# Optimization experiments

Hardware: AMD Instinct MI355X
Metric: run time of the kernel (lower is better)

Reference implementation:

```python
import jax, jax.numpy as jnp
import numpy as np

NUM_HEADS = 8
KEY_DIM = 32   # head_dim * attn_ratio(=1.0); head_dim = 256 // 8
SCALE = KEY_DIM ** -0.5


def qconv(x, w, groups, pad):
    """Quaternion (Hamilton product) conv. x: [B,C,4,H,W], w: [4,O,C//groups,kh,kw]."""
    B, C, Q, H, W = x.shape
    # fold the 4 quaternion components into the batch dim -> one conv per weight component
    xs = jnp.transpose(x, (0, 2, 1, 3, 4)).reshape(B * 4, C, H, W)
    ys = []
    for i in range(4):
        y = jax.lax.conv_general_dilated(
            xs, w[i], (1, 1), [(pad, pad), (pad, pad)],
            dimension_numbers=('NCHW', 'OIHW', 'NCHW'), feature_group_count=groups)
        ys.append(y.reshape(B, 4, y.shape[1], y.shape[2], y.shape[3]))
    yr, yi, yj, yk = ys  # y{w}[:, a] = conv(x_component_a, w_component_w)
    out_r = yr[:, 0] - yi[:, 1] - yj[:, 2] - yk[:, 3]
    out_i = yi[:, 0] + yr[:, 1] + yk[:, 2] - yj[:, 3]
    out_j = yj[:, 0] - yk[:, 1] + yr[:, 2] + yi[:, 3]
    out_k = yk[:, 0] + yj[:, 1] - yi[:, 2] + yr[:, 3]
    return jnp.stack([out_r, out_i, out_j, out_k], axis=2)  # [B,O,4,H,W]


def iqbn(x, gamma, beta, eps=1e-5):
    """Independent quaternion BN: per (channel, component) stats over (B,H,W)."""
    mean = x.mean(axis=(0, 3, 4), keepdims=True)
    var = x.var(axis=(0, 3, 4), keepdims=True)
    g = gamma[None, :, :, None, None]
    b = beta[None, :, :, None, None]
    return g * (x - mean) * jax.lax.rsqrt(var + eps) + b


def psablock(x, w_qkv, w_proj, w_pe, g_n, b_n, w_f1, g_f1, b_f1, w_f2, g_f2, b_f2):
    B, C, Q, H, W = x.shape
    N = H * W
    # --- QAttention ---
    qkv = qconv(x, w_qkv, 1, 0).reshape(B, NUM_HEADS, -1, 4, N)  # [B,nh,2kd+hd,4,N]
    q = qkv[:, :, :KEY_DIM]
    k = qkv[:, :, KEY_DIM:2 * KEY_DIM]
    v = qkv[:, :, 2 * KEY_DIM:]
    # channel attention: gram over spatial tokens N, softmax over channel dim d
    attn = jnp.einsum('bhcqn,bhdqn->bhqcd', q, k) * SCALE
    attn = jax.nn.softmax(attn, axis=-1)
    o = jnp.einsum('bhqcd,bhdqn->bhcqn', attn, v).reshape(B, C, 4, H, W)
    o = o + qconv(o, w_pe, C // 4, 1)   # depthwise-style 3x3 positional conv
    o = qconv(o, w_proj, 1, 0)
    o = iqbn(o, g_n, b_n)
    x = x + o  # shortcut
    # --- conv FFN ---
    f = qconv(x, w_f1, 1, 0)
    f = jax.nn.relu(iqbn(f, g_f1, b_f1))
    f = qconv(f, w_f2, 1, 0)
    f = iqbn(f, g_f2, b_f2)
    return x + f  # shortcut


def setup_inputs() -> dict:
    key = jax.random.key(0)
    ks = jax.random.split(key, 6)
    C, S = 256, 64
    return {
        'x': jax.random.normal(ks[0], (4, C, 4, S, S), jnp.float32),
        'w_qkv': jax.random.normal(ks[1], (4, 3 * C, C, 1, 1), jnp.float32) * 0.05,
        'w_proj': jax.random.normal(ks[2], (4, C, C, 1, 1), jnp.float32) * 0.05,
        'w_pe': jax.random.normal(ks[3], (4, C, 4, 3, 3), jnp.float32) * 0.05,
        'g_n': jnp.ones((C, 4), jnp.float32),
        'b_n': jnp.zeros((C, 4), jnp.float32),
        'w_f1': jax.random.normal(ks[4], (4, 2 * C, C, 1, 1), jnp.float32) * 0.05,
        'g_f1': jnp.ones((2 * C, 4), jnp.float32),
        'b_f1': jnp.zeros((2 * C, 4), jnp.float32),
        'w_f2': jax.random.normal(ks[5], (4, C, 2 * C, 1, 1), jnp.float32) * 0.05,
        'g_f2': jnp.ones((C, 4), jnp.float32),
        'b_f2': jnp.zeros((C, 4), jnp.float32),
    }


def reference(x, w_qkv, w_proj, w_pe, g_n, b_n, w_f1, g_f1, b_f1, w_f2, g_f2, b_f2):
    return psablock(x, w_qkv, w_proj, w_pe, g_n, b_n, w_f1, g_f1, b_f1, w_f2, g_f2, b_f2)
```

## Files before the change

### kernel.cpp

```cpp
#include <hip/hip_runtime.h>

typedef unsigned short u16;
typedef __bf16 bf16x8 __attribute__((ext_vector_type(8)));
typedef float f32x4 __attribute__((ext_vector_type(4)));

typedef const __attribute__((address_space(1))) void gv_t;
typedef __attribute__((address_space(3))) void lv_t;

__device__ __forceinline__ float b2f(u16 u) {
    union { unsigned int i; float f; } v; v.i = ((unsigned int)u) << 16; return v.f;
}
__device__ __forceinline__ u16 f2b(float f) {
    union { unsigned int i; float f; } v; v.f = f;
    unsigned int b = v.i;
    return (u16)((b + 0x7FFFu + ((b >> 16) & 1u)) >> 16);
}

__constant__ int   c_qidx[16] = {0,1,2,3, 1,0,3,2, 2,3,0,1, 3,2,1,0};
__constant__ float c_qsgn[16] = {1,-1,-1,-1, 1,1,1,-1, 1,-1,1,1, 1,1,-1,1};

__device__ __forceinline__ void frag_decode(long i, int KT, int& m, int& k) {
    int j = (int)(i & 7), r16 = (int)((i >> 3) & 15);
    int quad = (int)((i >> 7) & 3), frag = (int)((i >> 9) & 7);
    long t2 = i >> 12;
    int ktile = (int)(t2 % KT), mtile = (int)(t2 / KT);
    m = mtile * 128 + frag * 16 + r16;
    k = ktile * 32 + quad * 8 + j;
}
__device__ __forceinline__ u16 weff(const float* __restrict__ w, int OC, int Cin, int m, int k) {
    int o = m >> 2, p = m & 3, c = k >> 2, q = k & 3, pq = (p << 2) | q;
    return f2b(c_qsgn[pq] * w[c_qidx[pq] * OC + o * Cin + c]);
}

__global__ void build_weights(const float* __restrict__ wqkv, const float* __restrict__ wproj,
                              const float* __restrict__ wf1, const float* __restrict__ wf2,
                              const float* __restrict__ wpe,
                              u16* __restrict__ Wq, u16* __restrict__ Wp, u16* __restrict__ W1,
                              u16* __restrict__ W2, float* __restrict__ Wpe_eff)
{
    long i = (long)blockIdx.x * 256 + threadIdx.x;
    int m, k;
    if (i < 3145728L) {
        frag_decode(i, 32, m, k);
        Wq[i] = weff(wqkv, 196608, 256, m, k);
        return;
    }
    i -= 3145728L;
    if (i < 1048576L) {
        frag_decode(i, 32, m, k);
        Wp[i] = weff(wproj, 65536, 256, m, k);
        return;
    }
    i -= 1048576L;
    if (i < 2097152L) {
        frag_decode(i, 32, m, k);
        W1[i] = weff(wf1, 131072, 256, m, k);
        return;
    }
    i -= 2097152L;
    if (i < 2097152L) {
        frag_decode(i, 64, m, k);
        W2[i] = weff(wf2, 131072, 512, m, k);
        return;
    }
    i -= 2097152L;
    if (i < 147456L) {
        int g = (int)(i / 2304), r = (int)(i % 2304);
        int tap = r >> 8, r2 = r & 255;
        int fi = r2 >> 4, of = r2 & 15;
        int ol = of >> 2, p = of & 3, ci = fi >> 2, q = fi & 3, pq = (p << 2) | q;
        Wpe_eff[i] = c_qsgn[pq] * wpe[c_qidx[pq] * 9216 + (g * 4 + ol) * 36 + ci * 9 + tap];
    }
}

__global__ void zero_f(float* __restrict__ a)
{
    a[blockIdx.x * 256 + threadIdx.x] = 0.f;
}

__global__ __launch_bounds__(256) void cast_tr(const float* __restrict__ x, u16* __restrict__ Xt)
{
    int b = blockIdx.z, mt = blockIdx.y * 64, nt = blockIdx.x * 64;
    __shared__ u16 tl[64][66];
    int t = threadIdx.x, sub = t >> 4, c4 = (t & 15) * 4;
#pragma unroll
    for (int rr = 0; rr < 4; rr++) {
        int row = rr * 16 + sub;
        float4 v = *(const float4*)(x + ((long)b * 1024 + mt + row) * 4096 + nt + c4);
        uint2 pk;
        pk.x = (unsigned int)f2b(v.x) | ((unsigned int)f2b(v.y) << 16);
        pk.y = (unsigned int)f2b(v.z) | ((unsigned int)f2b(v.w) << 16);
        *(uint2*)(&tl[row][c4]) = pk;
    }
    __syncthreads();
#pragma unroll
    for (int rr = 0; rr < 4; rr++) {
        int row = rr * 16 + sub;
        uint2 o;
        o.x = (unsigned int)tl[c4][row] | ((unsigned int)tl[c4 + 1][row] << 16);
        o.y = (unsigned int)tl[c4 + 2][row] | ((unsigned int)tl[c4 + 3][row] << 16);
        *(uint2*)(Xt + ((long)b * 4096 + nt + row) * 1024 + mt + c4) = o;
    }
}

__device__ __forceinline__ void gl16(const u16* g, u16* l) {
    __builtin_amdgcn_global_load_lds((gv_t*)g, (lv_t*)l, 16, 0, 0);
}

template<int QM>
__device__ __forceinline__ void load_a(const u16* aS, bf16x8 (&afr)[4][2]) {
#pragma unroll
    for (int f = 0; f < 4; f++)
#pragma unroll
        for (int kk = 0; kk < 2; kk++)
            afr[f][kk] = *(const bf16x8*)(aS + (kk * 8 + QM * 4 + f) * 512);
}
template<int QN>
__device__ __forceinline__ void load_b(const u16* bS, bf16x8 (&bfr)[2][2]) {
#pragma unroll
    for (int g = 0; g < 2; g++)
#pragma unroll
        for (int kk = 0; kk < 2; kk++)
            bfr[g][kk] = *(const bf16x8*)(bS + (QN * 2 + g) * 1024 + kk * 512);
}
template<int QM, int QN>
__device__ __forceinline__ void mf16(const bf16x8 (&afr)[4][2], const bf16x8 (&bfr)[2][2],
                                     f32x4 (&acc)[8][4]) {
    __builtin_amdgcn_s_setprio(1);
#pragma unroll
    for (int f = 0; f < 4; f++)
#pragma unroll
        for (int g = 0; g < 2; g++)
#pragma unroll
            for (int kk = 0; kk < 2; kk++)
                acc[QM * 4 + f][QN * 2 + g] = __builtin_amdgcn_mfma_f32_16x16x32_bf16(
                    afr[f][kk], bfr[g][kk], acc[QM * 4 + f][QN * 2 + g], 0, 0, 0);
    __builtin_amdgcn_s_setprio(0);
}

template<bool TROUT>
__global__ __launch_bounds__(512, 2) void gemm256(
    const u16* __restrict__ A, const u16* __restrict__ Bt, u16* __restrict__ C,
    int M, int N, int K, long strideB, long strideC)
{
    __shared__ __align__(16) u16 smem[65536];
    const int t = threadIdx.x;
    const int b = blockIdx.z;
    const int m0 = blockIdx.y * 256, n0 = blockIdx.x * 256;
    const int l = t & 63, w = t >> 6;
    const int wr = w >> 2, wc = w & 3;
    const int quad = l >> 4, r16 = l & 15;
    const int KT32 = K >> 5, NT = K >> 6;
    const u16* Bb = Bt + (long)b * strideB;

    const u16* aB0 = A + (long)(2 * blockIdx.y) * KT32 * 4096 + t * 8;
    const u16* aB1 = aB0 + (long)KT32 * 4096;
    const int rowS = (w >> 1) * 16 + r16;
    const int colS = (w & 1) * 32 + quad * 8;
    const u16* bB0 = Bb + (long)(n0 + rowS) * K + colS;
    const u16* bB1 = bB0 + (long)128 * K;
    const long bStep = (long)64 * K;

#define STAGE_A(ktv, h) { \
    const u16* s_ = ((h) ? aB1 : aB0) + (long)(ktv) * 8192; \
    u16* d_ = smem + (((ktv) & 1) * 32768) + (h) * 8192 + t * 8; \
    gl16(s_, d_); gl16(s_ + 4096, d_ + 4096); }
#define STAGE_B(ktv, h) { \
    const u16* s_ = ((h) ? bB1 : bB0) + (ktv) * 64; \
    u16* d_ = smem + (((ktv) & 1) * 32768) + 16384 + (h) * 8192 + t * 8; \
    gl16(s_, d_); gl16(s_ + bStep, d_ + 4096); }
#define STAGE_TILE(ktv) { STAGE_A(ktv, 0); STAGE_A(ktv, 1); STAGE_B(ktv, 0); STAGE_B(ktv, 1); }

    STAGE_TILE(0);

    f32x4 acc[8][4];
#pragma unroll
    for (int i = 0; i < 8; i++)
#pragma unroll
        for (int j = 0; j < 4; j++) acc[i][j] = (f32x4){0.f, 0.f, 0.f, 0.f};

    for (int kt = 0; kt < NT; ++kt) {
        const int so = (kt & 1) * 32768;
        const u16* aS = smem + so + wr * 8192 + l * 8;
        const u16* bS = smem + so + 16384 + wc * 4096 + l * 8;
        bf16x8 afr[4][2], bfr[2][2];

        if (kt + 1 < NT) {
            STAGE_TILE(kt + 1);
            asm volatile("s_waitcnt vmcnt(8)" ::: "memory");
        } else {
            asm volatile("s_waitcnt vmcnt(0)" ::: "memory");
        }
        __builtin_amdgcn_s_barrier();

        load_a<0>(aS, afr);
        load_b<0>(bS, bfr);
        mf16<0, 0>(afr, bfr, acc);
        load_b<1>(bS, bfr);
        mf16<0, 1>(afr, bfr, acc);
        load_a<1>(aS, afr);
        mf16<1, 1>(afr, bfr, acc);
        load_b<0>(bS, bfr);
        mf16<1, 0>(afr, bfr, acc);

        __builtin_amdgcn_s_barrier();
    }
#undef STAGE_A
#undef STAGE_B
#undef STAGE_TILE

    if (!TROUT) {
        u16* Cb = C + (long)b * strideC;
#pragma unroll
        for (int i = 0; i < 8; i++)
#pragma unroll
            for (int j = 0; j < 4; j++) {
                int mm = m0 + wr * 128 + i * 16 + quad * 4;
                int nn = n0 + wc * 64 + j * 16 + r16;
#pragma unroll
                for (int r = 0; r < 4; r++)
                    Cb[(long)(mm + r) * N + nn] = f2b(acc[i][j][r]);
            }
    } else {
        u16* Ct = smem;
        u16* Cb = C + (long)b * strideC;
#pragma unroll
        for (int h = 0; h < 2; h++) {
            __syncthreads();
            if ((wc >> 1) == h) {
#pragma unroll
                for (int i = 0; i < 8; i++)
#pragma unroll
                    for (int j = 0; j < 4; j++) {
                        int nn = (wc & 1) * 64 + j * 16 + r16;
                        int mm = wr * 128 + i * 16 + quad * 4;
                        ushort4 pk;
                        pk.x = f2b(acc[i][j][0]); pk.y = f2b(acc[i][j][1]);
                        pk.z = f2b(acc[i][j][2]); pk.w = f2b(acc[i][j][3]);
                        *(ushort4*)(Ct + nn * 264 + mm) = pk;
                    }
            }
            __syncthreads();
#pragma unroll
            for (int e = 0; e < 8; e++) {
                int idx = e * 512 + t;
                int n = idx >> 5, m8 = (idx & 31) * 8;
                uint4 v = *(const uint4*)(Ct + n * 264 + m8);
                *(uint4*)(Cb + (long)(n0 + h * 128 + n) * M + m0 + m8) = v;
            }
        }
    }
}

__global__ __launch_bounds__(256) void attn_s(const u16* __restrict__ QKV, float* __restrict__ S)
{
    const int chunk = blockIdx.x, bhp = blockIdx.y;
    const int bi = bhp >> 5, h = (bhp >> 2) & 7, p = bhp & 3;
    const long rs = 16384;
    const u16* base = QKV + (long)bi * (3072L * 4096) + (long)(h * 384 + p) * 4096;
    const int t = threadIdx.x, l = t & 63, w = t >> 6;
    const int quad = l >> 4, r16 = l & 15;
    __shared__ float Sred[4][32][32];

    f32x4 acc[2][2];
#pragma unroll
    for (int i = 0; i < 2; i++)
#pragma unroll
        for (int j = 0; j < 2; j++) acc[i][j] = (f32x4){0.f, 0.f, 0.f, 0.f};

    const int nb = chunk * 1024 + w * 256 + quad * 8;
    for (int kk = 0; kk < 256; kk += 32) {
        long off = nb + kk;
        bf16x8 q0 = *(const bf16x8*)(base + (long)r16 * rs + off);
        bf16x8 q1 = *(const bf16x8*)(base + (long)(16 + r16) * rs + off);
        bf16x8 k0 = *(const bf16x8*)(base + (long)(32 + r16) * rs + off);
        bf16x8 k1 = *(const bf16x8*)(base + (long)(48 + r16) * rs + off);
        acc[0][0] = __builtin_amdgcn_mfma_f32_16x16x32_bf16(q0, k0, acc[0][0], 0, 0, 0);
        acc[0][1] = __builtin_amdgcn_mfma_f32_16x16x32_bf16(q0, k1, acc[0][1], 0, 0, 0);
        acc[1][0] = __builtin_amdgcn_mfma_f32_16x16x32_bf16(q1, k0, acc[1][0], 0, 0, 0);
        acc[1][1] = __builtin_amdgcn_mfma_f32_16x16x32_bf16(q1, k1, acc[1][1], 0, 0, 0);
    }
#pragma unroll
    for (int i = 0; i < 2; i++)
#pragma unroll
        for (int j = 0; j < 2; j++)
#pragma unroll
            for (int r = 0; r < 4; r++)
                Sred[w][i * 16 + quad * 4 + r][j * 16 + r16] = acc[i][j][r];
    __syncthreads();
    for (int e = t; e < 1024; e += 256) {
        int c = e >> 5, d = e & 31;
        float v = Sred[0][c][d] + Sred[1][c][d] + Sred[2][c][d] + Sred[3][c][d];
        atomicAdd(&S[(long)bhp * 1024 + e], v);
    }
}

__global__ __launch_bounds__(64) void attn_soft(float* __restrict__ S)
{
    const int bhp = blockIdx.x, t = threadIdx.x;
    if (t >= 32) return;
    float* row = S + (long)bhp * 1024 + t * 32;
    float r[32];
    float mx = -1e30f;
#pragma unroll
    for (int d = 0; d < 32; d++) { r[d] = row[d] * 0.17677669529663687f; mx = fmaxf(mx, r[d]); }
    float sum = 0.f;
#pragma unroll
    for (int d = 0; d < 32; d++) { r[d] = __expf(r[d] - mx); sum += r[d]; }
    float inv = 1.f / sum;
#pragma unroll
    for (int d = 0; d < 32; d++) row[d] = r[d] * inv;
}

__global__ __launch_bounds__(256) void attn_pv(const u16* __restrict__ QKV, const float* __restrict__ S,
                                               u16* __restrict__ O)
{
    const int ns = blockIdx.x * 512, bhp = blockIdx.y;
    const int bi = bhp >> 5, h = (bhp >> 2) & 7, p = bhp & 3;
    const long rs = 16384;
    const u16* base = QKV + (long)bi * (3072L * 4096) + (long)(h * 384 + p) * 4096;
    const int t = threadIdx.x;
    __shared__ float Pl[1024];
    for (int e = t; e < 1024; e += 256) Pl[e] = S[(long)bhp * 1024 + e];
    __syncthreads();

    float v[32][2];
#pragma unroll
    for (int d = 0; d < 32; d++) {
        unsigned int u = *(const unsigned int*)(base + (long)(64 + d) * rs + ns + 2 * t);
        v[d][0] = b2f((u16)u); v[d][1] = b2f((u16)(u >> 16));
    }
    u16* Ob = O + (long)bi * (1024L * 4096) + (long)(h * 128 + p) * 4096;
    for (int c = 0; c < 32; c++) {
        float s0 = 0.f, s1 = 0.f;
        const float4* prow = (const float4*)(&Pl[c * 32]);
#pragma unroll
        for (int dq = 0; dq < 8; dq++) {
            float4 pv = prow[dq];
            s0 = fmaf(pv.x, v[4*dq+0][0], s0); s1 = fmaf(pv.x, v[4*dq+0][1], s1);
            s0 = fmaf(pv.y, v[4*dq+1][0], s0); s1 = fmaf(pv.y, v[4*dq+1][1], s1);
            s0 = fmaf(pv.z, v[4*dq+2][0], s0); s1 = fmaf(pv.z, v[4*dq+2][1], s1);
            s0 = fmaf(pv.w, v[4*dq+3][0], s0); s1 = fmaf(pv.w, v[4*dq+3][1], s1);
        }
        *(unsigned int*)(Ob + (long)c * 16384 + ns + 2 * t) =
            (unsigned int)f2b(s0) | ((unsigned int)f2b(s1) << 16);
    }
}

__global__ __launch_bounds__(256) void pe_kernel(const u16* __restrict__ Oin,
                                                 const float* __restrict__ Wpe,
                                                 u16* __restrict__ O2t)
{
    const int tile = blockIdx.x, g = blockIdx.y, bi = blockIdx.z;
    const int y0 = (tile >> 2) * 16, x0 = (tile & 3) * 16;
    __shared__ float tin[16][324];
    const int t = threadIdx.x;
    const u16* Ob = Oin + (long)bi * (1024L * 4096) + (long)(g * 16) * 4096;
    for (int e = t; e < 16 * 324; e += 256) {
        int f = e / 324, rem = e % 324;
        int yy = rem / 18 - 1 + y0, xx = rem % 18 - 1 + x0;
        float v = 0.f;
        if (yy >= 0 && yy < 64 && xx >= 0 && xx < 64)
            v = b2f(Ob[(long)f * 4096 + yy * 64 + xx]);
        tin[f][rem] = v;
    }
    __syncthreads();
    const int y = t >> 4, x = t & 15;
    float acc[16];
#pragma unroll
    for (int of = 0; of < 16; of++) acc[of] = tin[of][(y + 1) * 18 + (x + 1)];
    const float* Wg = Wpe + g * 2304;
    for (int dy = 0; dy < 3; dy++)
        for (int dx = 0; dx < 3; dx++) {
            int off = (y + dy) * 18 + (x + dx);
            int tap = dy * 3 + dx;
            for (int fi = 0; fi < 16; fi++) {
                float v = tin[fi][off];
                const float* wp = Wg + (tap * 16 + fi) * 16;
#pragma unroll
                for (int of = 0; of < 16; of++) acc[of] = fmaf(wp[of], v, acc[of]);
            }
        }
    long n = (long)(y0 + y) * 64 + (x0 + x);
    unsigned int* op = (unsigned int*)(O2t + ((long)bi * 4096 + n) * 1024 + g * 16);
#pragma unroll
    for (int u = 0; u < 8; u++)
        op[u] = (unsigned int)f2b(acc[2 * u]) | ((unsigned int)f2b(acc[2 * u + 1]) << 16);
}

__global__ __launch_bounds__(256) void bn_stats(const u16* __restrict__ X, float* __restrict__ stats, int M)
{
    const int m = blockIdx.x, t = threadIdx.x;
    float s = 0.f, ss = 0.f;
    for (int b = 0; b < 4; b++) {
        const u16* rowp = X + ((long)b * M + m) * 4096;
        for (int pass = 0; pass < 2; pass++) {
            uint4 uv = *(const uint4*)(rowp + pass * 2048 + t * 8);
            unsigned int wsa[4] = {uv.x, uv.y, uv.z, uv.w};
#pragma unroll
            for (int u = 0; u < 4; u++) {
                float v0 = b2f((u16)wsa[u]), v1 = b2f((u16)(wsa[u] >> 16));
                s += v0 + v1; ss += v0 * v0 + v1 * v1;
            }
        }
    }
    __shared__ float rs[4], rss[4];
    for (int o = 32; o > 0; o >>= 1) { s += __shfl_down(s, o); ss += __shfl_down(ss, o); }
    if ((t & 63) == 0) { rs[t >> 6] = s; rss[t >> 6] = ss; }
    __syncthreads();
    if (t == 0) {
        float S = rs[0] + rs[1] + rs[2] + rs[3];
        float SS = rss[0] + rss[1] + rss[2] + rss[3];
        float mean = S * (1.f / 16384.f);
        float var = SS * (1.f / 16384.f) - mean * mean;
        stats[2 * m] = mean;
        stats[2 * m + 1] = rsqrtf(var + 1e-5f);
    }
}

__global__ __launch_bounds__(256) void bn_add_tr(const float* __restrict__ x, const u16* __restrict__ P,
    const float* __restrict__ stats, const float* __restrict__ gamma, const float* __restrict__ beta,
    u16* __restrict__ X1t)
{
    int b = blockIdx.z, mt = blockIdx.y * 64, nt = blockIdx.x * 64;
    __shared__ u16 tl[64][66];
    int t = threadIdx.x, sub = t >> 4, c4 = (t & 15) * 4;
#pragma unroll
    for (int rr = 0; rr < 4; rr++) {
        int row = rr * 16 + sub, m = mt + row;
        float gm = gamma[m] * stats[2 * m + 1];
        float bs = beta[m] - gm * stats[2 * m];
        long gi = ((long)b * 1024 + m) * 4096 + nt + c4;
        float4 xv = *(const float4*)(x + gi);
        uint2 pv = *(const uint2*)(P + gi);
        uint2 pk;
        pk.x = (unsigned int)f2b(xv.x + fmaf(gm, b2f((u16)pv.x), bs)) |
               ((unsigned int)f2b(xv.y + fmaf(gm, b2f((u16)(pv.x >> 16)), bs)) << 16);
        pk.y = (unsigned int)f2b(xv.z + fmaf(gm, b2f((u16)pv.y), bs)) |
               ((unsigned int)f2b(xv.w + fmaf(gm, b2f((u16)(pv.y >> 16)), bs)) << 16);
        *(uint2*)(&tl[row][c4]) = pk;
    }
    __syncthreads();
#pragma unroll
    for (int rr = 0; rr < 4; rr++) {
        int row = rr * 16 + sub;
        uint2 o;
        o.x = (unsigned int)tl[c4][row] | ((unsigned int)tl[c4 + 1][row] << 16);
        o.y = (unsigned int)tl[c4 + 2][row] | ((unsigned int)tl[c4 + 3][row] << 16);
        *(uint2*)(X1t + ((long)b * 4096 + nt + row) * 1024 + mt + c4) = o;
    }
}

__global__ __launch_bounds__(256) void bn_stats_col(const u16* __restrict__ Xp, float* __restrict__ accum)
{
    const int t = threadIdx.x;
    const int f0 = t * 8;
    float s[8], ss[8];
#pragma unroll
    for (int u = 0; u < 8; u++) { s[u] = 0.f; ss[u] = 0.f; }
    const u16* base = Xp + (long)blockIdx.x * 128 * 2048;
    for (int r = 0; r < 128; r++) {
        uint4 uv = *(const uint4*)(base + (long)r * 2048 + f0);
        unsigned int wsa[4] = {uv.x, uv.y, uv.z, uv.w};
#pragma unroll
        for (int u = 0; u < 4; u++) {
            float v0 = b2f((u16)wsa[u]), v1 = b2f((u16)(wsa[u] >> 16));
            s[2*u] += v0;   ss[2*u]   += v0 * v0;
            s[2*u+1] += v1; ss[2*u+1] += v1 * v1;
        }
    }
#pragma unroll
    for (int u = 0; u < 8; u++) {
        atomicAdd(&accum[f0 + u], s[u]);
        atomicAdd(&accum[2048 + f0 + u], ss[u]);
    }
}

__global__ __launch_bounds__(256) void bn_relu_ip(u16* __restrict__ Xp, const float* __restrict__ accum,
    const float* __restrict__ gamma, const float* __restrict__ beta)
{
    long i = ((long)blockIdx.x * 256 + threadIdx.x) * 8;
    int f = (int)(i & 2047);
    uint4 uv = *(const uint4*)(Xp + i);
    unsigned int wsa[4] = {uv.x, uv.y, uv.z, uv.w};
    unsigned int ov[4];
#pragma unroll
    for (int u = 0; u < 4; u++) {
        unsigned int o = 0;
#pragma unroll
        for (int h = 0; h < 2; h++) {
            int ff = f + 2 * u + h;
            float S = accum[ff], SS = accum[2048 + ff];
            float mean = S * (1.f / 16384.f);
            float var = SS * (1.f / 16384.f) - mean * mean;
            float g = gamma[ff] * rsqrtf(var + 1e-5f);
            float bb = beta[ff] - g * mean;
            float xv = b2f((u16)(wsa[u] >> (16 * h)));
            float v = fmaxf(fmaf(g, xv, bb), 0.f);
            o |= ((unsigned int)f2b(v)) << (16 * h);
        }
        ov[u] = o;
    }
    *(uint4*)(Xp + i) = *(uint4*)ov;
}

__global__ __launch_bounds__(256) void final_tr(const u16* __restrict__ X1t, const u16* __restrict__ F2,
    const float* __restrict__ stats, const float* __restrict__ gamma, const float* __restrict__ beta,
    float* __restrict__ out)
{
    int b = blockIdx.z, mt = blockIdx.y * 64, nt = blockIdx.x * 64;
    __shared__ u16 tl[64][66];
    int t = threadIdx.x, sub = t >> 4, c4 = (t & 15) * 4;
#pragma unroll
    for (int rr = 0; rr < 4; rr++) {
        int row = rr * 16 + sub;
        uint2 v = *(const uint2*)(X1t + ((long)b * 4096 + nt + row) * 1024 + mt + c4);
        *(uint2*)(&tl[row][c4]) = v;
    }
    __syncthreads();
#pragma unroll
    for (int rr = 0; rr < 4; rr++) {
        int row = rr * 16 + sub, m = mt + row;
        float gm = gamma[m] * stats[2 * m + 1];
        float bs = beta[m] - gm * stats[2 * m];
        long gi = ((long)b * 1024 + m) * 4096 + nt + c4;
        uint2 f = *(const uint2*)(F2 + gi);
        float4 o;
        o.x = b2f(tl[c4][row])     + fmaf(gm, b2f((u16)f.x), bs);
        o.y = b2f(tl[c4 + 1][row]) + fmaf(gm, b2f((u16)(f.x >> 16)), bs);
        o.z = b2f(tl[c4 + 2][row]) + fmaf(gm, b2f((u16)f.y), bs);
        o.w = b2f(tl[c4 + 3][row]) + fmaf(gm, b2f((u16)(f.y >> 16)), bs);
        *(float4*)(out + gi) = o;
    }
}

extern "C" void kernel_launch(void* const* d_in, const int* in_sizes, int n_in,
                              void* d_out, int out_size, void* d_ws, size_t ws_size,
                              hipStream_t stream)
{
    const float* x     = (const float*)d_in[0];
    const float* wqkv  = (const float*)d_in[1];
    const float* wproj = (const float*)d_in[2];
    const float* wpe   = (const float*)d_in[3];
    const float* g_n   = (const float*)d_in[4];
    const float* b_n   = (const float*)d_in[5];
    const float* wf1   = (const float*)d_in[6];
    const float* g_f1  = (const float*)d_in[7];
    const float* b_f1  = (const float*)d_in[8];
    const float* wf2   = (const float*)d_in[9];
    const float* g_f2  = (const float*)d_in[10];
    const float* b_f2  = (const float*)d_in[11];
    float* out = (float*)d_out;
    char* ws = (char*)d_ws;

    u16*   Wq      = (u16*)(ws + 0);
    u16*   Wp      = (u16*)(ws + 6291456);
    u16*   W1      = (u16*)(ws + 8388608);
    u16*   W2      = (u16*)(ws + 12582912);
    float* Wpe_eff = (float*)(ws + 16777216);
    float* st1     = (float*)(ws + 17367040);
    float* accum2  = (float*)(ws + 17375232);
    float* Sbuf    = (float*)(ws + 17391616);
    float* st3     = (float*)(ws + 17915904);
    u16*   QKV = (u16*)(ws + 17924096);
    u16*   O2t = (u16*)(ws + 17924096);
    u16*   X1t = (u16*)(ws + 17924096);
    u16*   P   = (u16*)(ws + 51478528);
    u16*   F1p = (u16*)(ws + 51478528);
    u16*   Xt  = (u16*)(ws + 118587392);
    u16*   Oat = (u16*)(ws + 118587392);
    u16*   F2  = (u16*)(ws + 118587392);

    zero_f<<<528, 256, 0, stream>>>(accum2);
    build_weights<<<33344, 256, 0, stream>>>(wqkv, wproj, wf1, wf2, wpe, Wq, Wp, W1, W2, Wpe_eff);
    cast_tr<<<dim3(64, 16, 4), 256, 0, stream>>>(x, Xt);
    gemm256<false><<<dim3(16, 12, 4), 512, 0, stream>>>(Wq, Xt, QKV, 3072, 4096, 1024, 4096L * 1024, 3072L * 4096);
    attn_s<<<dim3(4, 128), 256, 0, stream>>>(QKV, Sbuf);
    attn_soft<<<128, 64, 0, stream>>>(Sbuf);
    attn_pv<<<dim3(8, 128), 256, 0, stream>>>(QKV, Sbuf, Oat);
    pe_kernel<<<dim3(16, 64, 4), 256, 0, stream>>>(Oat, Wpe_eff, O2t);
    gemm256<false><<<dim3(16, 4, 4), 512, 0, stream>>>(Wp, O2t, P, 1024, 4096, 1024, 4096L * 1024, 1024L * 4096);
    bn_stats<<<1024, 256, 0, stream>>>(P, st1, 1024);
    bn_add_tr<<<dim3(64, 16, 4), 256, 0, stream>>>(x, P, st1, g_n, b_n, X1t);
    gemm256<true><<<dim3(16, 8, 4), 512, 0, stream>>>(W1, X1t, F1p, 2048, 4096, 1024, 4096L * 1024, 4096L * 2048);
    bn_stats_col<<<128, 256, 0, stream>>>(F1p, accum2);
    bn_relu_ip<<<16384, 256, 0, stream>>>(F1p, accum2, g_f1, b_f1);
    gemm256<false><<<dim3(16, 4, 4), 512, 0, stream>>>(W2, F1p, F2, 1024, 4096, 2048, 4096L * 2048, 1024L * 4096);
    bn_stats<<<1024, 256, 0, stream>>>(F2, st3, 1024);
    final_tr<<<dim3(64, 16, 4), 256, 0, stream>>>(X1t, F2, st3, g_f2, b_f2, out);
}
```

Measured before the change: 698.0 us.

## Software-pipeline LDS fragment reads across k-tiles in 256x256 GEMM

```diff
diff --git a/kernel.cpp b/kernel.cpp
--- a/kernel.cpp
+++ b/kernel.cpp
@@ -105,37 +105,6 @@
 
 __device__ __forceinline__ void gl16(const u16* g, u16* l) {
     __builtin_amdgcn_global_load_lds((gv_t*)g, (lv_t*)l, 16, 0, 0);
-}
-
-template<int QM>
-__device__ __forceinline__ void load_a(const u16* aS, bf16x8 (&afr)[4][2]) {
-#pragma unroll
-    for (int f = 0; f < 4; f++)
-#pragma unroll
-        for (int kk = 0; kk < 2; kk++)
-            afr[f][kk] = *(const bf16x8*)(aS + (kk * 8 + QM * 4 + f) * 512);
-}
-template<int QN>
-__device__ __forceinline__ void load_b(const u16* bS, bf16x8 (&bfr)[2][2]) {
-#pragma unroll
-    for (int g = 0; g < 2; g++)
-#pragma unroll
-        for (int kk = 0; kk < 2; kk++)
-            bfr[g][kk] = *(const bf16x8*)(bS + (QN * 2 + g) * 1024 + kk * 512);
-}
-template<int QM, int QN>
-__device__ __forceinline__ void mf16(const bf16x8 (&afr)[4][2], const bf16x8 (&bfr)[2][2],
-                                     f32x4 (&acc)[8][4]) {
-    __builtin_amdgcn_s_setprio(1);
-#pragma unroll
-    for (int f = 0; f < 4; f++)
-#pragma unroll
-        for (int g = 0; g < 2; g++)
-#pragma unroll
-            for (int kk = 0; kk < 2; kk++)
-                acc[QM * 4 + f][QN * 2 + g] = __builtin_amdgcn_mfma_f32_16x16x32_bf16(
-                    afr[f][kk], bfr[g][kk], acc[QM * 4 + f][QN * 2 + g], 0, 0, 0);
-    __builtin_amdgcn_s_setprio(0);
 }
 
 template<bool TROUT>
@@ -151,15 +120,18 @@
     const int wr = w >> 2, wc = w & 3;
     const int quad = l >> 4, r16 = l & 15;
     const int KT32 = K >> 5, NT = K >> 6;
-    const u16* Bb = Bt + (long)b * strideB;
+    const u16* BbG = Bt + (long)b * strideB;
 
     const u16* aB0 = A + (long)(2 * blockIdx.y) * KT32 * 4096 + t * 8;
     const u16* aB1 = aB0 + (long)KT32 * 4096;
     const int rowS = (w >> 1) * 16 + r16;
     const int colS = (w & 1) * 32 + quad * 8;
-    const u16* bB0 = Bb + (long)(n0 + rowS) * K + colS;
+    const u16* bB0 = BbG + (long)(n0 + rowS) * K + colS;
     const u16* bB1 = bB0 + (long)128 * K;
     const long bStep = (long)64 * K;
+
+    const int aOff = wr * 8192 + l * 8;
+    const int bOff = 16384 + wc * 4096 + l * 8;
 
 #define STAGE_A(ktv, h) { \
     const u16* s_ = ((h) ? aB1 : aB0) + (long)(ktv) * 8192; \
@@ -171,43 +143,66 @@
     gl16(s_, d_); gl16(s_ + bStep, d_ + 4096); }
 #define STAGE_TILE(ktv) { STAGE_A(ktv, 0); STAGE_A(ktv, 1); STAGE_B(ktv, 0); STAGE_B(ktv, 1); }
 
+#define RD_A(dst, sb, QM) { \
+    const u16* p_ = smem + (sb) + aOff; \
+    _Pragma("unroll") for (int f_ = 0; f_ < 4; f_++) \
+    _Pragma("unroll") for (int kk_ = 0; kk_ < 2; kk_++) \
+        dst[f_][kk_] = *(const bf16x8*)(p_ + (kk_ * 8 + (QM) * 4 + f_) * 512); }
+#define RD_B(dst, sb, QN) { \
+    const u16* p_ = smem + (sb) + bOff; \
+    _Pragma("unroll") for (int g_ = 0; g_ < 2; g_++) \
+    _Pragma("unroll") for (int kk_ = 0; kk_ < 2; kk_++) \
+        dst[g_][kk_] = *(const bf16x8*)(p_ + ((QN) * 2 + g_) * 1024 + kk_ * 512); }
+#define MF(QM, Ar, QN, Br) { \
+    __builtin_amdgcn_s_setprio(1); \
+    _Pragma("unroll") for (int f_ = 0; f_ < 4; f_++) \
+    _Pragma("unroll") for (int g_ = 0; g_ < 2; g_++) \
+    _Pragma("unroll") for (int kk_ = 0; kk_ < 2; kk_++) \
+        acc[(QM) * 4 + f_][(QN) * 2 + g_] = __builtin_amdgcn_mfma_f32_16x16x32_bf16( \
+            Ar[f_][kk_], Br[g_][kk_], acc[(QM) * 4 + f_][(QN) * 2 + g_], 0, 0, 0); \
+    __builtin_amdgcn_s_setprio(0); }
+
+    f32x4 acc[8][4];
+#pragma unroll
+    for (int i = 0; i < 8; i++)
+#pragma unroll
+        for (int j = 0; j < 4; j++) acc[i][j] = (f32x4){0.f, 0.f, 0.f, 0.f};
+
+    bf16x8 RA0[4][2], RA1[4][2], RB0[2][2], RB1[2][2];
+
     STAGE_TILE(0);
-
-    f32x4 acc[8][4];
-#pragma unroll
-    for (int i = 0; i < 8; i++)
-#pragma unroll
-        for (int j = 0; j < 4; j++) acc[i][j] = (f32x4){0.f, 0.f, 0.f, 0.f};
+    asm volatile("s_waitcnt vmcnt(0)" ::: "memory");
+    __builtin_amdgcn_s_barrier();
+    RD_A(RA0, 0, 0);
+    RD_B(RB0, 0, 0);
 
     for (int kt = 0; kt < NT; ++kt) {
-        const int so = (kt & 1) * 32768;
-        const u16* aS = smem + so + wr * 8192 + l * 8;
-        const u16* bS = smem + so + 16384 + wc * 4096 + l * 8;
-        bf16x8 afr[4][2], bfr[2][2];
-
-        if (kt + 1 < NT) {
-            STAGE_TILE(kt + 1);
-            asm volatile("s_waitcnt vmcnt(8)" ::: "memory");
-        } else {
-            asm volatile("s_waitcnt vmcnt(0)" ::: "memory");
-        }
+        const int so  = (kt & 1) * 32768;
+        const int so2 = so ^ 32768;
+        const bool st = (kt + 1 < NT);
+
+        if (st) STAGE_TILE(kt + 1);
+        RD_B(RB1, so, 1);
+        __builtin_amdgcn_sched_barrier(0);
+        MF(0, RA0, 0, RB0);
+        RD_A(RA1, so, 1);
+        __builtin_amdgcn_sched_barrier(0);
+        MF(0, RA0, 1, RB1);
+        __builtin_amdgcn_sched_barrier(0);
+        MF(1, RA1, 0, RB0);
+        asm volatile("s_waitcnt vmcnt(0)" ::: "memory");
         __builtin_amdgcn_s_barrier();
-
-        load_a<0>(aS, afr);
-        load_b<0>(bS, bfr);
-        mf16<0, 0>(afr, bfr, acc);
-        load_b<1>(bS, bfr);
-        mf16<0, 1>(afr, bfr, acc);
-        load_a<1>(aS, afr);
-        mf16<1, 1>(afr, bfr, acc);
-        load_b<0>(bS, bfr);
-        mf16<1, 0>(afr, bfr, acc);
-
+        if (st) { RD_A(RA0, so2, 0); RD_B(RB0, so2, 0); }
+        __builtin_amdgcn_sched_barrier(0);
+        MF(1, RA1, 1, RB1);
         __builtin_amdgcn_s_barrier();
     }
 #undef STAGE_A
 #undef STAGE_B
 #undef STAGE_TILE
+#undef RD_A
+#undef RD_B
+#undef MF
 
     if (!TROUT) {
         u16* Cb = C + (long)b * strideC;
```

After: 718.4 us. 1.03x slower.

## Fuse BN statistics into GEMM epilogues and softmax into attn_pv

Applied to the files above, without the earlier changes.

```diff
diff --git a/kernel.cpp b/kernel.cpp
--- a/kernel.cpp
+++ b/kernel.cpp
@@ -138,10 +138,10 @@
     __builtin_amdgcn_s_setprio(0);
 }
 
-template<bool TROUT>
+template<bool TROUT, bool STATS>
 __global__ __launch_bounds__(512, 2) void gemm256(
     const u16* __restrict__ A, const u16* __restrict__ Bt, u16* __restrict__ C,
-    int M, int N, int K, long strideB, long strideC)
+    int M, int N, int K, long strideB, long strideC, float* __restrict__ ST, int Mstat)
 {
     __shared__ __align__(16) u16 smem[65536];
     const int t = threadIdx.x;
@@ -208,6 +208,30 @@
 #undef STAGE_A
 #undef STAGE_B
 #undef STAGE_TILE
+
+    if constexpr (STATS) {
+#pragma unroll
+        for (int i = 0; i < 8; i++)
+#pragma unroll
+            for (int r = 0; r < 4; r++) {
+                float s = 0.f, ss = 0.f;
+#pragma unroll
+                for (int j = 0; j < 4; j++) {
+                    float v = acc[i][j][r];
+                    s += v; ss += v * v;
+                }
+#pragma unroll
+                for (int o = 1; o < 16; o <<= 1) {
+                    s  += __shfl_xor(s, o, 64);
+                    ss += __shfl_xor(ss, o, 64);
+                }
+                if (r16 == 0) {
+                    int mm = m0 + wr * 128 + i * 16 + quad * 4 + r;
+                    atomicAdd(&ST[mm], s);
+                    atomicAdd(&ST[Mstat + mm], ss);
+                }
+            }
+    }
 
     if (!TROUT) {
         u16* Cb = C + (long)b * strideC;
@@ -295,23 +319,6 @@
     }
 }
 
-__global__ __launch_bounds__(64) void attn_soft(float* __restrict__ S)
-{
-    const int bhp = blockIdx.x, t = threadIdx.x;
-    if (t >= 32) return;
-    float* row = S + (long)bhp * 1024 + t * 32;
-    float r[32];
-    float mx = -1e30f;
-#pragma unroll
-    for (int d = 0; d < 32; d++) { r[d] = row[d] * 0.17677669529663687f; mx = fmaxf(mx, r[d]); }
-    float sum = 0.f;
-#pragma unroll
-    for (int d = 0; d < 32; d++) { r[d] = __expf(r[d] - mx); sum += r[d]; }
-    float inv = 1.f / sum;
-#pragma unroll
-    for (int d = 0; d < 32; d++) row[d] = r[d] * inv;
-}
-
 __global__ __launch_bounds__(256) void attn_pv(const u16* __restrict__ QKV, const float* __restrict__ S,
                                                u16* __restrict__ O)
 {
@@ -322,6 +329,19 @@
     const int t = threadIdx.x;
     __shared__ float Pl[1024];
     for (int e = t; e < 1024; e += 256) Pl[e] = S[(long)bhp * 1024 + e];
+    __syncthreads();
+    if (t < 32) {
+        float r[32];
+        float mx = -1e30f;
+#pragma unroll
+        for (int d = 0; d < 32; d++) { r[d] = Pl[t * 32 + d] * 0.17677669529663687f; mx = fmaxf(mx, r[d]); }
+        float sum = 0.f;
+#pragma unroll
+        for (int d = 0; d < 32; d++) { r[d] = __expf(r[d] - mx); sum += r[d]; }
+        float inv = 1.f / sum;
+#pragma unroll
+        for (int d = 0; d < 32; d++) Pl[t * 32 + d] = r[d] * inv;
+    }
     __syncthreads();
 
     float v[32][2];
@@ -388,38 +408,8 @@
         op[u] = (unsigned int)f2b(acc[2 * u]) | ((unsigned int)f2b(acc[2 * u + 1]) << 16);
 }
 
-__global__ __launch_bounds__(256) void bn_stats(const u16* __restrict__ X, float* __restrict__ stats, int M)
-{
-    const int m = blockIdx.x, t = threadIdx.x;
-    float s = 0.f, ss = 0.f;
-    for (int b = 0; b < 4; b++) {
-        const u16* rowp = X + ((long)b * M + m) * 4096;
-        for (int pass = 0; pass < 2; pass++) {
-            uint4 uv = *(const uint4*)(rowp + pass * 2048 + t * 8);
-            unsigned int wsa[4] = {uv.x, uv.y, uv.z, uv.w};
-#pragma unroll
-            for (int u = 0; u < 4; u++) {
-                float v0 = b2f((u16)wsa[u]), v1 = b2f((u16)(wsa[u] >> 16));
-                s += v0 + v1; ss += v0 * v0 + v1 * v1;
-            }
-        }
-    }
-    __shared__ float rs[4], rss[4];
-    for (int o = 32; o > 0; o >>= 1) { s += __shfl_down(s, o); ss += __shfl_down(ss, o); }
-    if ((t & 63) == 0) { rs[t >> 6] = s; rss[t >> 6] = ss; }
-    __syncthreads();
-    if (t == 0) {
-        float S = rs[0] + rs[1] + rs[2] + rs[3];
-        float SS = rss[0] + rss[1] + rss[2] + rss[3];
-        float mean = S * (1.f / 16384.f);
-        float var = SS * (1.f / 16384.f) - mean * mean;
-        stats[2 * m] = mean;
-        stats[2 * m + 1] = rsqrtf(var + 1e-5f);
-    }
-}
-
 __global__ __launch_bounds__(256) void bn_add_tr(const float* __restrict__ x, const u16* __restrict__ P,
-    const float* __restrict__ stats, const float* __restrict__ gamma, const float* __restrict__ beta,
+    const float* __restrict__ ST, const float* __restrict__ gamma, const float* __restrict__ beta,
     u16* __restrict__ X1t)
 {
     int b = blockIdx.z, mt = blockIdx.y * 64, nt = blockIdx.x * 64;
@@ -428,8 +418,11 @@
 #pragma unroll
     for (int rr = 0; rr < 4; rr++) {
         int row = rr * 16 + sub, m = mt + row;
-        float gm = gamma[m] * stats[2 * m + 1];
-        float bs = beta[m] - gm * stats[2 * m];
+        float s = ST[m], ss = ST[1024 + m];
+        float mean = s * (1.f / 16384.f);
+        float var = ss * (1.f / 16384.f) - mean * mean;
+        float gm = gamma[m] * rsqrtf(var + 1e-5f);
+        float bs = beta[m] - gm * mean;
         long gi = ((long)b * 1024 + m) * 4096 + nt + c4;
         float4 xv = *(const float4*)(x + gi);
         uint2 pv = *(const uint2*)(P + gi);
@@ -448,31 +441,6 @@
         o.x = (unsigned int)tl[c4][row] | ((unsigned int)tl[c4 + 1][row] << 16);
         o.y = (unsigned int)tl[c4 + 2][row] | ((unsigned int)tl[c4 + 3][row] << 16);
         *(uint2*)(X1t + ((long)b * 4096 + nt + row) * 1024 + mt + c4) = o;
-    }
-}
-
-__global__ __launch_bounds__(256) void bn_stats_col(const u16* __restrict__ Xp, float* __restrict__ accum)
-{
-    const int t = threadIdx.x;
-    const int f0 = t * 8;
-    float s[8], ss[8];
-#pragma unroll
-    for (int u = 0; u < 8; u++) { s[u] = 0.f; ss[u] = 0.f; }
-    const u16* base = Xp + (long)blockIdx.x * 128 * 2048;
-    for (int r = 0; r < 128; r++) {
-        uint4 uv = *(const uint4*)(base + (long)r * 2048 + f0);
-        unsigned int wsa[4] = {uv.x, uv.y, uv.z, uv.w};
-#pragma unroll
-        for (int u = 0; u < 4; u++) {
-            float v0 = b2f((u16)wsa[u]), v1 = b2f((u16)(wsa[u] >> 16));
-            s[2*u] += v0;   ss[2*u]   += v0 * v0;
-            s[2*u+1] += v1; ss[2*u+1] += v1 * v1;
-        }
-    }
-#pragma unroll
-    for (int u = 0; u < 8; u++) {
-        atomicAdd(&accum[f0 + u], s[u]);
-        atomicAdd(&accum[2048 + f0 + u], ss[u]);
     }
 }
 
@@ -505,7 +473,7 @@
 }
 
 __global__ __launch_bounds__(256) void final_tr(const u16* __restrict__ X1t, const u16* __restrict__ F2,
-    const float* __restrict__ stats, const float* __restrict__ gamma, const float* __restrict__ beta,
+    const float* __restrict__ ST, const float* __restrict__ gamma, const float* __restrict__ beta,
     float* __restrict__ out)
 {
     int b = blockIdx.z, mt = blockIdx.y * 64, nt = blockIdx.x * 64;
@@ -521,8 +489,11 @@
 #pragma unroll
     for (int rr = 0; rr < 4; rr++) {
         int row = rr * 16 + sub, m = mt + row;
-        float gm = gamma[m] * stats[2 * m + 1];
-        float bs = beta[m] - gm * stats[2 * m];
+        float s = ST[m], ss = ST[1024 + m];
+        float mean = s * (1.f / 16384.f);
+        float var = ss * (1.f / 16384.f) - mean * mean;
+        float gm = gamma[m] * rsqrtf(var + 1e-5f);
+        float bs = beta[m] - gm * mean;
         long gi = ((long)b * 1024 + m) * 4096 + nt + c4;
         uint2 f = *(const uint2*)(F2 + gi);
         float4 o;
@@ -559,9 +530,10 @@
     u16*   W2      = (u16*)(ws + 12582912);
     float* Wpe_eff = (float*)(ws + 16777216);
     float* st1     = (float*)(ws + 17367040);
-    float* accum2  = (float*)(ws + 17375232);
-    float* Sbuf    = (float*)(ws + 17391616);
-    float* st3     = (float*)(ws + 17915904);
+    float* st3     = (float*)(ws + 17375232);
+    float* accum2  = (float*)(ws + 17383424);
+    float* Sbuf    = (float*)(ws + 17399808);
+    float* st_zero = st1;
     u16*   QKV = (u16*)(ws + 17924096);
     u16*   O2t = (u16*)(ws + 17924096);
     u16*   X1t = (u16*)(ws + 17924096);
@@ -571,21 +543,17 @@
     u16*   Oat = (u16*)(ws + 118587392);
     u16*   F2  = (u16*)(ws + 118587392);
 
-    zero_f<<<528, 256, 0, stream>>>(accum2);
+    zero_f<<<544, 256, 0, stream>>>(st_zero);
     build_weights<<<33344, 256, 0, stream>>>(wqkv, wproj, wf1, wf2, wpe, Wq, Wp, W1, W2, Wpe_eff);
     cast_tr<<<dim3(64, 16, 4), 256, 0, stream>>>(x, Xt);
-    gemm256<false><<<dim3(16, 12, 4), 512, 0, stream>>>(Wq, Xt, QKV, 3072, 4096, 1024, 4096L * 1024, 3072L * 4096);
+    gemm256<false, false><<<dim3(16, 12, 4), 512, 0, stream>>>(Wq, Xt, QKV, 3072, 4096, 1024, 4096L * 1024, 3072L * 4096, nullptr, 0);
     attn_s<<<dim3(4, 128), 256, 0, stream>>>(QKV, Sbuf);
-    attn_soft<<<128, 64, 0, stream>>>(Sbuf);
     attn_pv<<<dim3(8, 128), 256, 0, stream>>>(QKV, Sbuf, Oat);
     pe_kernel<<<dim3(16, 64, 4), 256, 0, stream>>>(Oat, Wpe_eff, O2t);
-    gemm256<false><<<dim3(16, 4, 4), 512, 0, stream>>>(Wp, O2t, P, 1024, 4096, 1024, 4096L * 1024, 1024L * 4096);
-    bn_stats<<<1024, 256, 0, stream>>>(P, st1, 1024);
+    gemm256<false, true><<<dim3(16, 4, 4), 512, 0, stream>>>(Wp, O2t, P, 1024, 4096, 1024, 4096L * 1024, 1024L * 4096, st1, 1024);
     bn_add_tr<<<dim3(64, 16, 4), 256, 0, stream>>>(x, P, st1, g_n, b_n, X1t);
-    gemm256<true><<<dim3(16, 8, 4), 512, 0, stream>>>(W1, X1t, F1p, 2048, 4096, 1024, 4096L * 1024, 4096L * 2048);
-    bn_stats_col<<<128, 256, 0, stream>>>(F1p, accum2);
+    gemm256<true, true><<<dim3(16, 8, 4), 512, 0, stream>>>(W1, X1t, F1p, 2048, 4096, 1024, 4096L * 1024, 4096L * 2048, accum2, 2048);
     bn_relu_ip<<<16384, 256, 0, stream>>>(F1p, accum2, g_f1, b_f1);
-    gemm256<false><<<dim3(16, 4, 4), 512, 0, stream>>>(W2, F1p, F2, 1024, 4096, 2048, 4096L * 2048, 1024L * 4096);
-    bn_stats<<<1024, 256, 0, stream>>>(F2, st3, 1024);
+    gemm256<false, true><<<dim3(16, 4, 4), 512, 0, stream>>>(W2, F1p, F2, 1024, 4096, 2048, 4096L * 2048, 1024L * 4096, st3, 1024);
     final_tr<<<dim3(64, 16, 4), 256, 0, stream>>>(X1t, F2, st3, g_f2, b_f2, out);
 }
```

After: 788.0 us. 12.9% more time.

## Interleave GEMM global staging with MFMA phases and fuse softmax into attn_pv

Applied to the files above, without the earlier changes.

```diff
diff --git a/kernel.cpp b/kernel.cpp
--- a/kernel.cpp
+++ b/kernel.cpp
@@ -137,6 +137,13 @@
                     afr[f][kk], bfr[g][kk], acc[QM * 4 + f][QN * 2 + g], 0, 0, 0);
     __builtin_amdgcn_s_setprio(0);
 }
+
+#define PHASE_SYNC() \
+    __builtin_amdgcn_sched_barrier(0); \
+    asm volatile("s_waitcnt vmcnt(4)" ::: "memory"); \
+    __builtin_amdgcn_s_barrier(); \
+    asm volatile("s_waitcnt lgkmcnt(0)" ::: "memory"); \
+    __builtin_amdgcn_sched_barrier(0);
 
 template<bool TROUT>
 __global__ __launch_bounds__(512, 2) void gemm256(
@@ -161,6 +168,9 @@
     const u16* bB1 = bB0 + (long)128 * K;
     const long bStep = (long)64 * K;
 
+    const int aOff = wr * 8192 + l * 8;
+    const int bOff = 16384 + wc * 4096 + l * 8;
+
 #define STAGE_A(ktv, h) { \
     const u16* s_ = ((h) ? aB1 : aB0) + (long)(ktv) * 8192; \
     u16* d_ = smem + (((ktv) & 1) * 32768) + (h) * 8192 + t * 8; \
@@ -169,45 +179,52 @@
     const u16* s_ = ((h) ? bB1 : bB0) + (ktv) * 64; \
     u16* d_ = smem + (((ktv) & 1) * 32768) + 16384 + (h) * 8192 + t * 8; \
     gl16(s_, d_); gl16(s_ + bStep, d_ + 4096); }
-#define STAGE_TILE(ktv) { STAGE_A(ktv, 0); STAGE_A(ktv, 1); STAGE_B(ktv, 0); STAGE_B(ktv, 1); }
-
-    STAGE_TILE(0);
 
     f32x4 acc[8][4];
 #pragma unroll
     for (int i = 0; i < 8; i++)
 #pragma unroll
         for (int j = 0; j < 4; j++) acc[i][j] = (f32x4){0.f, 0.f, 0.f, 0.f};
+
+    bf16x8 RA[4][2], RB0[2][2], RB1[2][2];
+
+    STAGE_B(0, 0); STAGE_A(0, 0); STAGE_B(0, 1); STAGE_A(0, 1);
+    STAGE_B(1, 0); STAGE_A(1, 0);
+    asm volatile("s_waitcnt vmcnt(4)" ::: "memory");
+    __builtin_amdgcn_s_barrier();
 
     for (int kt = 0; kt < NT; ++kt) {
         const int so = (kt & 1) * 32768;
-        const u16* aS = smem + so + wr * 8192 + l * 8;
-        const u16* bS = smem + so + 16384 + wc * 4096 + l * 8;
-        bf16x8 afr[4][2], bfr[2][2];
-
-        if (kt + 1 < NT) {
-            STAGE_TILE(kt + 1);
-            asm volatile("s_waitcnt vmcnt(8)" ::: "memory");
-        } else {
-            asm volatile("s_waitcnt vmcnt(0)" ::: "memory");
-        }
+        const u16* aS = smem + so + aOff;
+        const u16* bS = smem + so + bOff;
+        const int k1 = (kt + 1 < NT) ? kt + 1 : NT - 1;
+        const int k2 = (kt + 2 < NT) ? kt + 2 : NT - 1;
+
+        load_a<0>(aS, RA);
+        load_b<0>(bS, RB0);
+        STAGE_B(k1, 1);
+        PHASE_SYNC();
+        mf16<0, 0>(RA, RB0, acc);
         __builtin_amdgcn_s_barrier();
-
-        load_a<0>(aS, afr);
-        load_b<0>(bS, bfr);
-        mf16<0, 0>(afr, bfr, acc);
-        load_b<1>(bS, bfr);
-        mf16<0, 1>(afr, bfr, acc);
-        load_a<1>(aS, afr);
-        mf16<1, 1>(afr, bfr, acc);
-        load_b<0>(bS, bfr);
-        mf16<1, 0>(afr, bfr, acc);
-
+        load_b<1>(bS, RB1);
+        STAGE_A(k1, 1);
+        PHASE_SYNC();
+        mf16<0, 1>(RA, RB1, acc);
         __builtin_amdgcn_s_barrier();
-    }
+        load_a<1>(aS, RA);
+        STAGE_B(k2, 0);
+        PHASE_SYNC();
+        mf16<1, 1>(RA, RB1, acc);
+        __builtin_amdgcn_s_barrier();
+        STAGE_A(k2, 0);
+        PHASE_SYNC();
+        mf16<1, 0>(RA, RB0, acc);
+        __builtin_amdgcn_s_barrier();
+    }
+    asm volatile("s_waitcnt vmcnt(0)" ::: "memory");
+    __builtin_amdgcn_s_barrier();
 #undef STAGE_A
 #undef STAGE_B
-#undef STAGE_TILE
 
     if (!TROUT) {
         u16* Cb = C + (long)b * strideC;
@@ -251,6 +268,7 @@
         }
     }
 }
+#undef PHASE_SYNC
 
 __global__ __launch_bounds__(256) void attn_s(const u16* __restrict__ QKV, float* __restrict__ S)
 {
@@ -295,23 +313,6 @@
     }
 }
 
-__global__ __launch_bounds__(64) void attn_soft(float* __restrict__ S)
-{
-    const int bhp = blockIdx.x, t = threadIdx.x;
-    if (t >= 32) return;
-    float* row = S + (long)bhp * 1024 + t * 32;
-    float r[32];
-    float mx = -1e30f;
-#pragma unroll
-    for (int d = 0; d < 32; d++) { r[d] = row[d] * 0.17677669529663687f; mx = fmaxf(mx, r[d]); }
-    float sum = 0.f;
-#pragma unroll
-    for (int d = 0; d < 32; d++) { r[d] = __expf(r[d] - mx); sum += r[d]; }
-    float inv = 1.f / sum;
-#pragma unroll
-    for (int d = 0; d < 32; d++) row[d] = r[d] * inv;
-}
-
 __global__ __launch_bounds__(256) void attn_pv(const u16* __restrict__ QKV, const float* __restrict__ S,
                                                u16* __restrict__ O)
 {
@@ -322,6 +323,19 @@
     const int t = threadIdx.x;
     __shared__ float Pl[1024];
     for (int e = t; e < 1024; e += 256) Pl[e] = S[(long)bhp * 1024 + e];
+    __syncthreads();
+    if (t < 32) {
+        float r[32];
+        float mx = -1e30f;
+#pragma unroll
+        for (int d = 0; d < 32; d++) { r[d] = Pl[t * 32 + d] * 0.17677669529663687f; mx = fmaxf(mx, r[d]); }
+        float sum = 0.f;
+#pragma unroll
+        for (int d = 0; d < 32; d++) { r[d] = __expf(r[d] - mx); sum += r[d]; }
+        float inv = 1.f / sum;
+#pragma unroll
+        for (int d = 0; d < 32; d++) Pl[t * 32 + d] = r[d] * inv;
+    }
     __syncthreads();
 
     float v[32][2];
@@ -576,7 +590,6 @@
     cast_tr<<<dim3(64, 16, 4), 256, 0, stream>>>(x, Xt);
     gemm256<false><<<dim3(16, 12, 4), 512, 0, stream>>>(Wq, Xt, QKV, 3072, 4096, 1024, 4096L * 1024, 3072L * 4096);
     attn_s<<<dim3(4, 128), 256, 0, stream>>>(QKV, Sbuf);
-    attn_soft<<<128, 64, 0, stream>>>(Sbuf);
     attn_pv<<<dim3(8, 128), 256, 0, stream>>>(QKV, Sbuf, Oat);
     pe_kernel<<<dim3(16, 64, 4), 256, 0, stream>>>(Oat, Wpe_eff, O2t);
     gemm256<false><<<dim3(16, 4, 4), 512, 0, stream>>>(Wp, O2t, P, 1024, 4096, 1024, 4096L * 1024, 1024L * 4096);
```

Result: no change. 693.3 us (-0.7%).
